# Optimization experiments

Measured on AMD Instinct MI355X. Metric: run time of the kernel, lower is better.

## Reference

```python
import math
import jax, jax.numpy as jnp
import numpy as np

B, T, E, H, D = 2, 2048, 1024, 16, 64


def setup_inputs() -> dict:
    key = jax.random.key(0)
    ks = jax.random.split(key, 6)
    x = jax.random.normal(ks[0], (B, T, E), dtype=jnp.float32)
    wr = jax.random.normal(ks[1], (H, E, T), dtype=jnp.float32) * math.sqrt(2.0 / E)
    wvr_w = jax.random.normal(ks[2], (H * D, E), dtype=jnp.float32) * (1.0 / math.sqrt(E))
    wj_w = jax.random.normal(ks[3], (E, E), dtype=jnp.float32) * (1.0 / math.sqrt(E))
    gate = jnp.zeros((H, 2), dtype=jnp.float32)
    wo_w = jax.random.normal(ks[4], (E, H * D), dtype=jnp.float32) * (1.0 / math.sqrt(H * D))
    return {"x": x, "wr": wr, "wvr_w": wvr_w, "wj_w": wj_w, "gate": gate, "wo_w": wo_w}


def reference(x, wr, wvr_w, wj_w, gate, wo_w):
    B_, T_, E_ = x.shape
    H_ = gate.shape[0]
    D_ = wvr_w.shape[0] // H_
    sc = 1.0 / math.sqrt(D_)
    mask = jnp.triu(jnp.ones((T_, T_), dtype=bool), k=1)  # True above diagonal

    # --- RRP branch: score-based causal attention with per-head learned key scores ---
    rv = (x @ wvr_w.T).reshape(B_, T_, H_, D_).transpose(0, 2, 1, 3)  # [B,H,T,D]
    ra = jnp.einsum('bte,het->bht', x, wr[:, :, :T_]) * sc            # [B,H,T]
    ra = jnp.where(mask, -jnp.inf, ra[:, :, None, :])                 # [B,H,T,T]
    rrp_out = jax.nn.softmax(ra, axis=-1) @ rv                        # [B,H,T,D]

    # --- Janus branch: outer-product shared attention over echoed features ---
    echo = x @ wj_w.T                                                 # [B,T,E]
    eb = echo @ wj_w                                                  # F.linear(echo, W.T)
    sc2 = (x * eb).sum(-1) / math.sqrt(E_)                            # [B,T]
    ja = jnp.where(mask, -jnp.inf, sc2[:, :, None] * sc2[:, None, :]) # [B,T,T]
    ja = jax.nn.softmax(ja, axis=-1)
    jan_out = jnp.einsum('bst,bthd->bhsd', ja, echo.reshape(B_, T_, H_, D_))  # [B,H,T,D]

    # --- Gated fusion per head ---
    g = jax.nn.softmax(gate, axis=-1)                                 # [H,2]
    out = (g[:, 0][None, :, None, None] * rrp_out
           + g[:, 1][None, :, None, None] * jan_out)                  # [B,H,T,D]
    out = out.transpose(0, 2, 1, 3).reshape(B_, T_, H_ * D_)
    return out @ wo_w.T
```

## Files before the change

### kernel.cpp

```cpp
#include <hip/hip_runtime.h>
#include <hip/hip_bf16.h>
#include <stdint.h>

#define B_    2
#define T_    2048
#define E_    1024
#define H_    16
#define D_    64
#define NTOK  (B_*T_)

typedef unsigned short u16;
typedef short s16x8 __attribute__((ext_vector_type(8)));
typedef float f32x4 __attribute__((ext_vector_type(4)));

__device__ __forceinline__ u16 f2bf(float f) {
  uint32_t u = __float_as_uint(f);
  u += 0x7FFFu + ((u >> 16) & 1u);
  return (u16)(u >> 16);
}
__device__ __forceinline__ float bf2f(u16 h) {
  return __uint_as_float(((uint32_t)h) << 16);
}
__device__ __forceinline__ void split2(float v, u16 &h, u16 &l) {
  h = f2bf(v);
  l = f2bf(v - bf2f(h));
}

__device__ __forceinline__ void gload_lds16(const void* g, void* l) {
  void* gnc = const_cast<void*>(g);
  __builtin_amdgcn_global_load_lds(
      (__attribute__((address_space(1))) uint32_t*)gnc,
      (__attribute__((address_space(3))) uint32_t*)l, 16, 0, 0);
}

#define MFMA_BF16(accv, av, bv) \
  asm("v_mfma_f32_16x16x32_bf16 %0, %1, %2, %0" : "+v"(accv) : "v"(av), "v"(bv))

__global__ __launch_bounds__(256) void k_split(const float* __restrict__ in,
                                               u16* __restrict__ hi,
                                               u16* __restrict__ lo, int n4) {
  int i = blockIdx.x * 256 + threadIdx.x;
  if (i >= n4) return;
  float4 v = ((const float4*)in)[i];
  u16 h0,h1,h2,h3,l0,l1,l2,l3;
  split2(v.x,h0,l0); split2(v.y,h1,l1); split2(v.z,h2,l2); split2(v.w,h3,l3);
  ushort4 hv; hv.x=h0; hv.y=h1; hv.z=h2; hv.w=h3;
  ushort4 lv; lv.x=l0; lv.y=l1; lv.z=l2; lv.w=l3;
  ((ushort4*)hi)[i] = hv;
  ((ushort4*)lo)[i] = lv;
}

template<int BN>
__global__ __launch_bounds__(256) void gemm_nt_split(
    const u16* __restrict__ Ahi, const u16* __restrict__ Alo,
    const u16* __restrict__ Bhi, const u16* __restrict__ Blo,
    float* __restrict__ C0, float* __restrict__ C1, int Nsplit, int ldC,
    int M, int N, int K,
    long long sA, long long sB, long long sC, int causal) {
  constexpr int NJ = BN / 32;
  const int bz = blockIdx.z;
  Ahi += (size_t)bz * sA; Alo += (size_t)bz * sA;
  Bhi += (size_t)bz * sB; Blo += (size_t)bz * sB;
  C0  += (size_t)bz * sC; C1  += (size_t)bz * sC;

  const int m0 = blockIdx.y * 128;
  const int n0 = blockIdx.x * BN;
  const int tid  = threadIdx.x;
  const int lane = tid & 63;
  const int w    = tid >> 6;
  const int wm = w >> 1, wn = w & 1;
  const int kmax = causal ? ((m0 + 128 < K) ? (m0 + 128) : K) : K;

  __shared__ u16 sAhi[128*32], sAlo[128*32], sBhi[BN*32], sBlo[BN*32];

  const int r0 = tid >> 2;
  const int c0 = (tid & 3) * 8;
  const size_t arow  = (size_t)(m0 + r0) * K;
  const size_t arow2 = (size_t)(m0 + 64 + r0) * K;
  const size_t brow  = (size_t)(n0 + r0) * K;
  const size_t brow2 = (size_t)(n0 + 64 + r0) * K;
  const int ldso = r0 * 32 + c0;

  f32x4 acc[4][NJ] = {};

  for (int k0 = 0; k0 < kmax; k0 += 32) {
    const int kc = k0 + c0;
    gload_lds16(Ahi + arow  + kc, &sAhi[ldso]);
    gload_lds16(Ahi + arow2 + kc, &sAhi[64*32 + ldso]);
    gload_lds16(Alo + arow  + kc, &sAlo[ldso]);
    gload_lds16(Alo + arow2 + kc, &sAlo[64*32 + ldso]);
    gload_lds16(Bhi + brow  + kc, &sBhi[ldso]);
    gload_lds16(Blo + brow  + kc, &sBlo[ldso]);
    if constexpr (BN == 128) {
      gload_lds16(Bhi + brow2 + kc, &sBhi[64*32 + ldso]);
      gload_lds16(Blo + brow2 + kc, &sBlo[64*32 + ldso]);
    }
    __syncthreads();

    const int la = lane & 15;
    const int ka = (lane >> 4) * 8;
    s16x8 ah[4], al[4], bh[NJ], bl[NJ];
    #pragma unroll
    for (int i = 0; i < 4; ++i) {
      const int ar = (wm*64 + i*16 + la) * 32 + ka;
      ah[i] = *(const s16x8*)&sAhi[ar];
      al[i] = *(const s16x8*)&sAlo[ar];
    }
    #pragma unroll
    for (int j = 0; j < NJ; ++j) {
      const int br = (wn*(BN/2) + j*16 + la) * 32 + ka;
      bh[j] = *(const s16x8*)&sBhi[br];
      bl[j] = *(const s16x8*)&sBlo[br];
    }
    #pragma unroll
    for (int i = 0; i < 4; ++i) {
      #pragma unroll
      for (int j = 0; j < NJ; ++j) {
        MFMA_BF16(acc[i][j], al[i], bh[j]);
        MFMA_BF16(acc[i][j], ah[i], bl[j]);
        MFMA_BF16(acc[i][j], ah[i], bh[j]);
      }
    }
    __syncthreads();
  }

  asm volatile("s_nop 7\n\ts_nop 7\n\ts_nop 7" ::);

  const int cr = (lane >> 4) * 4;
  const int cc = lane & 15;
  float* Cb = (n0 >= Nsplit) ? C1 : C0;
  const int nbase = (n0 >= Nsplit) ? n0 - Nsplit : n0;
  #pragma unroll
  for (int i = 0; i < 4; ++i) {
    #pragma unroll
    for (int j = 0; j < NJ; ++j) {
      const size_t row = (size_t)(m0 + wm*64 + i*16 + cr);
      const int col = nbase + wn*(BN/2) + j*16 + cc;
      float* cp = Cb + row * ldC + col;
      cp[0]               = acc[i][j][0];
      cp[(size_t)ldC]     = acc[i][j][1];
      cp[(size_t)2*ldC]   = acc[i][j][2];
      cp[(size_t)3*ldC]   = acc[i][j][3];
    }
  }
}

__global__ __launch_bounds__(256) void k_sc2(const float* __restrict__ echo,
                                             float* __restrict__ sc2) {
  int tok  = blockIdx.x * 4 + (threadIdx.x >> 6);
  int lane = threadIdx.x & 63;
  const float4* p = (const float4*)(echo + (size_t)tok * E_);
  float s = 0.f;
  #pragma unroll
  for (int j = 0; j < 4; ++j) {
    float4 v = p[lane + j*64];
    s += v.x*v.x + v.y*v.y + v.z*v.z + v.w*v.w;
  }
  #pragma unroll
  for (int off = 32; off; off >>= 1) s += __shfl_xor(s, off);
  if (lane == 0) sc2[tok] = s * (1.0f/32.0f);
}

__global__ __launch_bounds__(256) void k_tsplit(const float* __restrict__ echo,
                                                u16* __restrict__ Thi,
                                                u16* __restrict__ Tlo) {
  __shared__ float tile[32][33];
  int b = blockIdx.z;
  int t0 = blockIdx.x * 32, e0 = blockIdx.y * 32;
  int lx = threadIdx.x & 31, ly = threadIdx.x >> 5;
  #pragma unroll
  for (int i = 0; i < 32; i += 8)
    tile[ly + i][lx] = echo[((size_t)b*T_ + t0 + ly + i) * E_ + e0 + lx];
  __syncthreads();
  #pragma unroll
  for (int i = 0; i < 32; i += 8) {
    float v = tile[lx][ly + i];
    size_t o = ((size_t)b*E_ + e0 + ly + i) * T_ + t0 + lx;
    u16 h, l; split2(v, h, l);
    Thi[o] = h; Tlo[o] = l;
  }
}

__global__ __launch_bounds__(256) void k_ra(const float* __restrict__ x,
                                            const float* __restrict__ wr,
                                            float* __restrict__ ra) {
  int t  = blockIdx.x * 256 + threadIdx.x;
  int h  = blockIdx.y;
  int ec = blockIdx.z;
  const float* wrp = wr + ((size_t)h * E_ + ec * 64) * T_ + t;
  const float* x0  = x + (size_t)t * E_ + ec * 64;
  const float* x1  = x0 + (size_t)T_ * E_;
  float a0 = 0.f, a1 = 0.f;
  #pragma unroll 16
  for (int e = 0; e < 64; ++e) {
    float w = wrp[(size_t)e * T_];
    a0 = fmaf(x0[e], w, a0);
    a1 = fmaf(x1[e], w, a1);
  }
  atomicAdd(&ra[(size_t)h * T_ + t], a0);
  atomicAdd(&ra[(size_t)(H_ + h) * T_ + t], a1);
}

__global__ __launch_bounds__(256) void k_rrp1(const float* __restrict__ ra,
    const float* __restrict__ rv, float* __restrict__ gmaxb,
    float* __restrict__ csnum, float* __restrict__ csden) {
  int bh = blockIdx.x;
  int b = bh >> 4, h = bh & 15;
  int tid = threadIdx.x;
  const float* rar = ra + (size_t)bh * T_;
  __shared__ float red[256];
  float mx = -1e30f;
  for (int t = tid; t < T_; t += 256) mx = fmaxf(mx, rar[t]);
  red[tid] = mx; __syncthreads();
  for (int s = 128; s > 0; s >>= 1) {
    if (tid < s) red[tid] = fmaxf(red[tid], red[tid + s]);
    __syncthreads();
  }
  float gm = red[0] * 0.125f;
  if (tid == 0) gmaxb[bh] = gm;
  int w = tid >> 6, lane = tid & 63;
  for (int c = w; c < 32; c += 4) {
    float num = 0.f, den = 0.f;
    int t0 = c * 64;
    const float* rvp = rv + ((size_t)b * T_ + t0) * E_ + h * 64 + lane;
    #pragma unroll 4
    for (int i = 0; i < 64; ++i) {
      float wt = __expf(fmaf(rar[t0 + i], 0.125f, -gm));
      num = fmaf(wt, rvp[(size_t)i * E_], num);
      den += wt;
    }
    csnum[((size_t)bh * 32 + c) * 64 + lane] = num;
    if (lane == 0) csden[bh * 32 + c] = den;
  }
}

__global__ __launch_bounds__(64) void k_rrp2(const float* __restrict__ ra,
    const float* __restrict__ rv, const float* __restrict__ gmaxb,
    const float* __restrict__ csnum, const float* __restrict__ csden,
    float* __restrict__ rrp) {
  int bh = blockIdx.x, c = blockIdx.y;
  int b = bh >> 4, h = bh & 15;
  int lane = threadIdx.x;
  float gm = gmaxb[bh];
  const float* rar = ra + (size_t)bh * T_;
  float num = 0.f, den = 0.f;
  for (int cc = 0; cc < c; ++cc) {
    num += csnum[((size_t)bh * 32 + cc) * 64 + lane];
    den += csden[bh * 32 + cc];
  }
  int t0 = c * 64;
  const float* rvp = rv  + ((size_t)b * T_ + t0) * E_ + h * 64 + lane;
  float*       op  = rrp + ((size_t)b * T_ + t0) * E_ + h * 64 + lane;
  for (int i = 0; i < 64; ++i) {
    float wt = __expf(fmaf(rar[t0 + i], 0.125f, -gm));
    num = fmaf(wt, rvp[(size_t)i * E_], num);
    den += wt;
    op[(size_t)i * E_] = num / den;
  }
}

__global__ __launch_bounds__(256) void k_pmax(const float* __restrict__ sc2,
                                              float* __restrict__ pmax) {
  int b = blockIdx.x;
  __shared__ float u[T_];
  int tid = threadIdx.x;
  for (int i = tid; i < T_; i += 256) u[i] = sc2[b*T_ + i];
  __syncthreads();
  for (int off = 1; off < T_; off <<= 1) {
    float v[8];
    #pragma unroll
    for (int k = 0; k < 8; ++k) {
      int i = tid + k*256;
      v[k] = (i >= off) ? fmaxf(u[i], u[i-off]) : u[i];
    }
    __syncthreads();
    #pragma unroll
    for (int k = 0; k < 8; ++k) u[tid + k*256] = v[k];
    __syncthreads();
  }
  for (int i = tid; i < T_; i += 256) pmax[b*T_ + i] = u[i];
}

__global__ __launch_bounds__(256) void k_jden(const float* __restrict__ sc2,
    const float* __restrict__ pmax, float* __restrict__ jm,
    float* __restrict__ jden) {
  int b = blockIdx.y;
  int s = blockIdx.x * 4 + (threadIdx.x >> 6);
  int lane = threadIdx.x & 63;
  const float* u = sc2 + b*T_;
  float a = u[s];
  float m = a * pmax[b*T_ + s];
  float d = 0.f;
  for (int t = lane; t <= s; t += 64) d += __expf(fmaf(a, u[t], -m));
  #pragma unroll
  for (int off = 32; off; off >>= 1) d += __shfl_xor(d, off);
  if (lane == 0) { jm[b*T_+s] = m; jden[b*T_+s] = d; }
}

__global__ __launch_bounds__(256) void k_pgen(const float* __restrict__ sc2,
    const float* __restrict__ jm, const float* __restrict__ jden,
    u16* __restrict__ Phi, u16* __restrict__ Plo) {
  int b = blockIdx.z;
  size_t base = ((size_t)blockIdx.x * 256 + threadIdx.x) * 8;
  int s  = (int)(base >> 11);
  int t0 = (int)(base & 2047);
  const float* u = sc2 + b*T_;
  float a = u[s];
  float m = jm[b*T_+s];
  float invd = 1.0f / jden[b*T_+s];
  u16 hh[8], ll[8];
  #pragma unroll
  for (int k = 0; k < 8; ++k) {
    int tt = t0 + k;
    float p = (tt <= s) ? __expf(fmaf(a, u[tt], -m)) * invd : 0.0f;
    split2(p, hh[k], ll[k]);
  }
  size_t o = ((size_t)b*T_ + s) * T_ + t0;
  ushort4 h0; h0.x=hh[0]; h0.y=hh[1]; h0.z=hh[2]; h0.w=hh[3];
  ushort4 h1; h1.x=hh[4]; h1.y=hh[5]; h1.z=hh[6]; h1.w=hh[7];
  ushort4 l0; l0.x=ll[0]; l0.y=ll[1]; l0.z=ll[2]; l0.w=ll[3];
  ushort4 l1; l1.x=ll[4]; l1.y=ll[5]; l1.z=ll[6]; l1.w=ll[7];
  *(ushort4*)(Phi + o)     = h0; *(ushort4*)(Phi + o + 4) = h1;
  *(ushort4*)(Plo + o)     = l0; *(ushort4*)(Plo + o + 4) = l1;
}

__global__ __launch_bounds__(256) void k_fuse(const float* __restrict__ rrp,
    const float* __restrict__ jan, const float* __restrict__ gate,
    u16* __restrict__ Fhi, u16* __restrict__ Flo) {
  int i = blockIdx.x * 256 + threadIdx.x;
  int h = (i & 255) >> 4;
  float g0 = gate[h*2], g1 = gate[h*2+1];
  float mg = fmaxf(g0, g1);
  float e0 = __expf(g0 - mg), e1 = __expf(g1 - mg);
  float inv = 1.0f / (e0 + e1);
  float w0 = e0 * inv, w1 = e1 * inv;
  float4 r = ((const float4*)rrp)[i];
  float4 j = ((const float4*)jan)[i];
  u16 hh[4], ll[4];
  split2(w0*r.x + w1*j.x, hh[0], ll[0]);
  split2(w0*r.y + w1*j.y, hh[1], ll[1]);
  split2(w0*r.z + w1*j.z, hh[2], ll[2]);
  split2(w0*r.w + w1*j.w, hh[3], ll[3]);
  ushort4 hv; hv.x=hh[0]; hv.y=hh[1]; hv.z=hh[2]; hv.w=hh[3];
  ushort4 lv; lv.x=ll[0]; lv.y=ll[1]; lv.z=ll[2]; lv.w=ll[3];
  ((ushort4*)Fhi)[i] = hv;
  ((ushort4*)Flo)[i] = lv;
}

extern "C" void kernel_launch(void* const* d_in, const int* in_sizes, int n_in,
                              void* d_out, int out_size, void* d_ws, size_t ws_size,
                              hipStream_t stream) {
  const float* x    = (const float*)d_in[0];
  const float* wr   = (const float*)d_in[1];
  const float* wvr  = (const float*)d_in[2];
  const float* wj   = (const float*)d_in[3];
  const float* gate = (const float*)d_in[4];
  const float* wo   = (const float*)d_in[5];
  float* out = (float*)d_out;

  char* p = (char*)d_ws;
  auto alloc = [&](size_t bytes) {
    char* r = p;
    p += (bytes + 255) & ~(size_t)255;
    return r;
  };
  u16* x_hi   = (u16*)alloc((size_t)NTOK*E_*2);
  u16* x_lo   = (u16*)alloc((size_t)NTOK*E_*2);
  u16* wvr_hi = (u16*)alloc((size_t)E_*E_*2);
  u16* wj_hi  = (u16*)alloc((size_t)E_*E_*2);
  u16* wvr_lo = (u16*)alloc((size_t)E_*E_*2);
  u16* wj_lo  = (u16*)alloc((size_t)E_*E_*2);
  u16* wo_hi  = (u16*)alloc((size_t)E_*E_*2);
  u16* wo_lo  = (u16*)alloc((size_t)E_*E_*2);
  float* rv   = (float*)alloc((size_t)NTOK*E_*4);
  float* echo = (float*)alloc((size_t)NTOK*E_*4);
  u16* p_lo   = (u16*)alloc((size_t)B_*T_*T_*2);
  u16* eT_hi  = (u16*)alloc((size_t)B_*E_*T_*2);
  u16* eT_lo  = (u16*)alloc((size_t)B_*E_*T_*2);
  float* sc2  = (float*)alloc((size_t)NTOK*4);
  float* ra   = (float*)alloc((size_t)B_*H_*T_*4);
  float* gmaxb= (float*)alloc(32*4);
  float* csnum= (float*)alloc((size_t)32*32*64*4);
  float* csden= (float*)alloc((size_t)32*32*4);
  float* pmaxv= (float*)alloc((size_t)NTOK*4);
  float* jm   = (float*)alloc((size_t)NTOK*4);
  float* jden = (float*)alloc((size_t)NTOK*4);
  float* rrp  = (float*)alloc((size_t)NTOK*E_*4);
  u16* f_hi   = (u16*)alloc((size_t)NTOK*E_*2);
  u16* f_lo   = (u16*)alloc((size_t)NTOK*E_*2);
  u16* p_hi = (u16*)echo;
  float* jan = rv;

  int n4;
  n4 = NTOK*E_/4; k_split<<<dim3((n4+255)/256),256,0,stream>>>(x,   x_hi,   x_lo,   n4);
  n4 = E_*E_/4;   k_split<<<dim3((n4+255)/256),256,0,stream>>>(wvr, wvr_hi, wvr_lo, n4);
                  k_split<<<dim3((n4+255)/256),256,0,stream>>>(wj,  wj_hi,  wj_lo,  n4);
                  k_split<<<dim3((n4+255)/256),256,0,stream>>>(wo,  wo_hi,  wo_lo,  n4);

  gemm_nt_split<128><<<dim3(16,32,1),256,0,stream>>>(
      x_hi, x_lo, wvr_hi, wvr_lo, rv, echo, E_, E_,
      NTOK, 2*E_, E_, 0,0,0, 0);

  k_sc2<<<dim3(NTOK/4),256,0,stream>>>(echo, sc2);
  k_tsplit<<<dim3(T_/32, E_/32, B_),256,0,stream>>>(echo, eT_hi, eT_lo);

  hipMemsetAsync(ra, 0, (size_t)B_*H_*T_*4, stream);
  k_ra<<<dim3(T_/256, H_, 16),256,0,stream>>>(x, wr, ra);

  k_rrp1<<<dim3(32),256,0,stream>>>(ra, rv, gmaxb, csnum, csden);
  k_rrp2<<<dim3(32,32),64,0,stream>>>(ra, rv, gmaxb, csnum, csden, rrp);

  k_pmax<<<dim3(B_),256,0,stream>>>(sc2, pmaxv);
  k_jden<<<dim3(T_/4, B_),256,0,stream>>>(sc2, pmaxv, jm, jden);
  k_pgen<<<dim3(T_*T_/2048, 1, B_),256,0,stream>>>(sc2, jm, jden, p_hi, p_lo);
  gemm_nt_split<64><<<dim3(16,16,2),256,0,stream>>>(
      p_hi, p_lo, eT_hi, eT_lo, jan, jan, 1<<30, E_,
      T_, E_, T_, (long long)T_*T_, (long long)E_*T_, (long long)T_*E_, 1);

  n4 = NTOK*E_/4;
  k_fuse<<<dim3(n4/256),256,0,stream>>>(rrp, jan, gate, f_hi, f_lo);
  gemm_nt_split<64><<<dim3(16,32,1),256,0,stream>>>(
      f_hi, f_lo, wo_hi, wo_lo, out, out, 1<<30, E_,
      NTOK, E_, E_, 0,0,0, 0);
}
```

Baseline: 535.9 us.

## Swizzle GEMM LDS layout, restage ra in shared memory, split rrp1 into parallel kernels

The split-bf16 GEMM now XOR-swizzles the K-chunk column used for global loads and LDS fragment reads, which is meant to reduce LDS bank conflicts. The ra projection kernel is rebuilt so x tiles are staged transposed in shared memory and reused across four heads, with a new grid (T/64, E/32, H/4). That grid issues many more atomic adds. The old single-phase rrp1, which ran only 32 blocks, is split into a gmax reduction kernel and a chunk-sum kernel with a 32x32 grid to expose more parallelism, at the cost of one extra launch.

Result: faster. 458.5 us (-14.5%).

```diff
diff --git a/kernel.cpp b/kernel.cpp
--- a/kernel.cpp
+++ b/kernel.cpp
@@ -74,12 +74,12 @@
   __shared__ u16 sAhi[128*32], sAlo[128*32], sBhi[BN*32], sBlo[BN*32];
 
   const int r0 = tid >> 2;
-  const int c0 = (tid & 3) * 8;
+  const int c0 = (((tid & 3) ^ ((tid >> 3) & 3)) * 8);
+  const int ldso = r0 * 32 + (tid & 3) * 8;
   const size_t arow  = (size_t)(m0 + r0) * K;
   const size_t arow2 = (size_t)(m0 + 64 + r0) * K;
   const size_t brow  = (size_t)(n0 + r0) * K;
   const size_t brow2 = (size_t)(n0 + 64 + r0) * K;
-  const int ldso = r0 * 32 + c0;
 
   f32x4 acc[4][NJ] = {};
 
@@ -98,17 +98,17 @@
     __syncthreads();
 
     const int la = lane & 15;
-    const int ka = (lane >> 4) * 8;
+    const int kap = (((lane >> 4) ^ ((lane >> 1) & 3)) * 8);
     s16x8 ah[4], al[4], bh[NJ], bl[NJ];
     #pragma unroll
     for (int i = 0; i < 4; ++i) {
-      const int ar = (wm*64 + i*16 + la) * 32 + ka;
+      const int ar = (wm*64 + i*16 + la) * 32 + kap;
       ah[i] = *(const s16x8*)&sAhi[ar];
       al[i] = *(const s16x8*)&sAlo[ar];
     }
     #pragma unroll
     for (int j = 0; j < NJ; ++j) {
-      const int br = (wn*(BN/2) + j*16 + la) * 32 + ka;
+      const int br = (wn*(BN/2) + j*16 + la) * 32 + kap;
       bh[j] = *(const s16x8*)&sBhi[br];
       bl[j] = *(const s16x8*)&sBlo[br];
     }
@@ -184,28 +184,38 @@
 __global__ __launch_bounds__(256) void k_ra(const float* __restrict__ x,
                                             const float* __restrict__ wr,
                                             float* __restrict__ ra) {
-  int t  = blockIdx.x * 256 + threadIdx.x;
-  int h  = blockIdx.y;
-  int ec = blockIdx.z;
-  const float* wrp = wr + ((size_t)h * E_ + ec * 64) * T_ + t;
-  const float* x0  = x + (size_t)t * E_ + ec * 64;
-  const float* x1  = x0 + (size_t)T_ * E_;
+  __shared__ float xs[2][32][65];
+  const int tid  = threadIdx.x;
+  const int lane = tid & 63;
+  const int t0 = blockIdx.x * 64;
+  const int e0 = blockIdx.y * 32;
+  const int h  = blockIdx.z * 4 + (tid >> 6);
+  #pragma unroll
+  for (int b = 0; b < 2; ++b)
+    #pragma unroll
+    for (int p = 0; p < 2; ++p) {
+      const int ee = (tid & 3) * 4 + p * 16;
+      const int tt = tid >> 2;
+      float4 v = *(const float4*)&x[((size_t)b*T_ + t0 + tt) * E_ + e0 + ee];
+      xs[b][ee+0][tt] = v.x; xs[b][ee+1][tt] = v.y;
+      xs[b][ee+2][tt] = v.z; xs[b][ee+3][tt] = v.w;
+    }
+  __syncthreads();
+  const float* wrp = wr + ((size_t)h * E_ + e0) * T_ + t0 + lane;
   float a0 = 0.f, a1 = 0.f;
-  #pragma unroll 16
-  for (int e = 0; e < 64; ++e) {
-    float w = wrp[(size_t)e * T_];
-    a0 = fmaf(x0[e], w, a0);
-    a1 = fmaf(x1[e], w, a1);
-  }
-  atomicAdd(&ra[(size_t)h * T_ + t], a0);
-  atomicAdd(&ra[(size_t)(H_ + h) * T_ + t], a1);
-}
-
-__global__ __launch_bounds__(256) void k_rrp1(const float* __restrict__ ra,
-    const float* __restrict__ rv, float* __restrict__ gmaxb,
-    float* __restrict__ csnum, float* __restrict__ csden) {
+  #pragma unroll 8
+  for (int e = 0; e < 32; ++e) {
+    float wv = wrp[(size_t)e * T_];
+    a0 = fmaf(xs[0][e][lane], wv, a0);
+    a1 = fmaf(xs[1][e][lane], wv, a1);
+  }
+  atomicAdd(&ra[(size_t)h * T_ + t0 + lane], a0);
+  atomicAdd(&ra[(size_t)(H_ + h) * T_ + t0 + lane], a1);
+}
+
+__global__ __launch_bounds__(256) void k_gmax(const float* __restrict__ ra,
+                                              float* __restrict__ gmaxb) {
   int bh = blockIdx.x;
-  int b = bh >> 4, h = bh & 15;
   int tid = threadIdx.x;
   const float* rar = ra + (size_t)bh * T_;
   __shared__ float red[256];
@@ -216,22 +226,28 @@
     if (tid < s) red[tid] = fmaxf(red[tid], red[tid + s]);
     __syncthreads();
   }
-  float gm = red[0] * 0.125f;
-  if (tid == 0) gmaxb[bh] = gm;
-  int w = tid >> 6, lane = tid & 63;
-  for (int c = w; c < 32; c += 4) {
-    float num = 0.f, den = 0.f;
-    int t0 = c * 64;
-    const float* rvp = rv + ((size_t)b * T_ + t0) * E_ + h * 64 + lane;
-    #pragma unroll 4
-    for (int i = 0; i < 64; ++i) {
-      float wt = __expf(fmaf(rar[t0 + i], 0.125f, -gm));
-      num = fmaf(wt, rvp[(size_t)i * E_], num);
-      den += wt;
-    }
-    csnum[((size_t)bh * 32 + c) * 64 + lane] = num;
-    if (lane == 0) csden[bh * 32 + c] = den;
-  }
+  if (tid == 0) gmaxb[bh] = red[0] * 0.125f;
+}
+
+__global__ __launch_bounds__(64) void k_csum(const float* __restrict__ ra,
+    const float* __restrict__ rv, const float* __restrict__ gmaxb,
+    float* __restrict__ csnum, float* __restrict__ csden) {
+  int bh = blockIdx.x, c = blockIdx.y;
+  int b = bh >> 4, h = bh & 15;
+  int lane = threadIdx.x;
+  float gm = gmaxb[bh];
+  const float* rar = ra + (size_t)bh * T_;
+  int t0 = c * 64;
+  const float* rvp = rv + ((size_t)b * T_ + t0) * E_ + h * 64 + lane;
+  float num = 0.f, den = 0.f;
+  #pragma unroll 4
+  for (int i = 0; i < 64; ++i) {
+    float wt = __expf(fmaf(rar[t0 + i], 0.125f, -gm));
+    num = fmaf(wt, rvp[(size_t)i * E_], num);
+    den += wt;
+  }
+  csnum[((size_t)bh * 32 + c) * 64 + lane] = num;
+  if (lane == 0) csden[bh * 32 + c] = den;
 }
 
 __global__ __launch_bounds__(64) void k_rrp2(const float* __restrict__ ra,
@@ -405,9 +421,10 @@
   k_tsplit<<<dim3(T_/32, E_/32, B_),256,0,stream>>>(echo, eT_hi, eT_lo);
 
   hipMemsetAsync(ra, 0, (size_t)B_*H_*T_*4, stream);
-  k_ra<<<dim3(T_/256, H_, 16),256,0,stream>>>(x, wr, ra);
-
-  k_rrp1<<<dim3(32),256,0,stream>>>(ra, rv, gmaxb, csnum, csden);
+  k_ra<<<dim3(T_/64, E_/32, H_/4),256,0,stream>>>(x, wr, ra);
+
+  k_gmax<<<dim3(32),256,0,stream>>>(ra, gmaxb);
+  k_csum<<<dim3(32,32),64,0,stream>>>(ra, rv, gmaxb, csnum, csden);
   k_rrp2<<<dim3(32,32),64,0,stream>>>(ra, rv, gmaxb, csnum, csden, rrp);
 
   k_pmax<<<dim3(B_),256,0,stream>>>(sc2, pmaxv);
```
